# Performance work log

Hardware: AMD Instinct MI355X
Metric: run time of the kernel (lower is better)

Reference implementation:

```python
import jax, jax.numpy as jnp
import numpy as np

B, S, H = 8, 1024, 1024
NH, DH = 16, 64
F_DIM, E, TOPK = 4096, 8, 2
EPS = 1e-5


def setup_inputs() -> dict:
    key = jax.random.key(0)
    ks = jax.random.split(key, 12)
    s = 0.02
    return {
        "x": jax.random.normal(ks[0], (B, S, H), jnp.float32),
        "ln1_w": jnp.ones((H,), jnp.float32),
        "ln1_b": jnp.zeros((H,), jnp.float32),
        "ln2_w": jnp.ones((H,), jnp.float32),
        "ln2_b": jnp.zeros((H,), jnp.float32),
        "in_proj_w": jax.random.normal(ks[1], (3 * H, H), jnp.float32) * s,
        "in_proj_b": jnp.zeros((3 * H,), jnp.float32),
        "out_proj_w": jax.random.normal(ks[2], (H, H), jnp.float32) * s,
        "out_proj_b": jnp.zeros((H,), jnp.float32),
        "gate_w": jax.random.normal(ks[3], (E, H), jnp.float32) * s,
        "gate_b": jnp.zeros((E,), jnp.float32),
        "w1": jax.random.normal(ks[4], (E, H, F_DIM), jnp.float32) * s,
        "b1": jnp.zeros((E, F_DIM), jnp.float32),
        "w2": jax.random.normal(ks[5], (E, F_DIM, H), jnp.float32) * s,
        "b2": jnp.zeros((E, H), jnp.float32),
    }


def _layernorm(x, w, b):
    mu = jnp.mean(x, axis=-1, keepdims=True)
    var = jnp.var(x, axis=-1, keepdims=True)
    return (x - mu) * jax.lax.rsqrt(var + EPS) * w + b


def reference(x, ln1_w, ln1_b, ln2_w, ln2_b, in_proj_w, in_proj_b,
              out_proj_w, out_proj_b, gate_w, gate_b, w1, b1, w2, b2):
    # --- attention sub-block ---
    xn = _layernorm(x, ln1_w, ln1_b)
    qkv = xn @ in_proj_w.T + in_proj_b                     # [B,S,3H]
    q, k, v = jnp.split(qkv, 3, axis=-1)
    q = q.reshape(B, S, NH, DH).transpose(0, 2, 1, 3)      # [B,NH,S,DH]
    k = k.reshape(B, S, NH, DH).transpose(0, 2, 1, 3)
    v = v.reshape(B, S, NH, DH).transpose(0, 2, 1, 3)
    scores = jnp.einsum("bhqd,bhkd->bhqk", q, k) / jnp.sqrt(jnp.float32(DH))
    attn = jax.nn.softmax(scores, axis=-1)
    ctx = jnp.einsum("bhqk,bhkd->bhqd", attn, v)
    ctx = ctx.transpose(0, 2, 1, 3).reshape(B, S, H)
    x = x + ctx @ out_proj_w.T + out_proj_b

    # --- MoE sub-block (dense compute-all-experts, top-k combine) ---
    xn2 = _layernorm(x, ln2_w, ln2_b)
    logits = xn2 @ gate_w.T + gate_b                       # [B,S,E]
    topk_vals, topk_idx = jax.lax.top_k(logits, TOPK)      # [B,S,K]
    probs = jax.nn.softmax(topk_vals, axis=-1)
    hid = jax.nn.gelu(jnp.einsum("bsh,ehf->bsef", xn2, w1) + b1, approximate=False)
    expert_out = jnp.einsum("bsef,efh->bseh", hid, w2) + b2  # [B,S,E,H]
    selected = jnp.take_along_axis(expert_out, topk_idx[..., None], axis=2)  # [B,S,K,H]
    moe_out = jnp.sum(probs[..., None] * selected, axis=2)
    return x + moe_out
```

## Files before the change

kernel.cpp:

```cpp
#include <hip/hip_runtime.h>
#include <math.h>

typedef unsigned short u16;
typedef short short8 __attribute__((ext_vector_type(8)));
typedef float f32x4 __attribute__((ext_vector_type(4)));
typedef unsigned short us4 __attribute__((ext_vector_type(4)));

#define NTOK 8192
#define NEXP 8

__device__ __forceinline__ u16 f2bf(float f) {
  union { float f; unsigned u; } v; v.f = f;
  unsigned r = v.u + 0x7FFFu + ((v.u >> 16) & 1u);
  return (u16)(r >> 16);
}
__device__ __forceinline__ float bf2f(u16 u) {
  union { unsigned u; float f; } v; v.u = ((unsigned)u) << 16; return v.f;
}
__device__ __forceinline__ void gload16(const u16* src, u16* ldsDst) {
  __builtin_amdgcn_global_load_lds(
    (const __attribute__((address_space(1))) unsigned int*)(const void*)src,
    (__attribute__((address_space(3))) unsigned int*)(void*)ldsDst, 16, 0, 0);
}

__global__ void cast_kernel(const float* __restrict__ in, u16* __restrict__ out, int n4) {
  int i = blockIdx.x * blockDim.x + threadIdx.x;
  if (i < n4) {
    float4 v = ((const float4*)in)[i];
    us4 o;
    o[0] = f2bf(v.x); o[1] = f2bf(v.y); o[2] = f2bf(v.z); o[3] = f2bf(v.w);
    ((us4*)out)[i] = o;
  }
}

__global__ void transpose_cast(const float* __restrict__ in, u16* __restrict__ out, int R, int C) {
  __shared__ float tile[64][65];
  const size_t eoff = (size_t)blockIdx.z * (size_t)R * (size_t)C;
  in += eoff; out += eoff;
  const int rb = blockIdx.y * 64, cb = blockIdx.x * 64;
  const int tid = threadIdx.x;
  const int lr4 = tid >> 4;
  const int lc4 = (tid & 15) * 4;
#pragma unroll
  for (int p = 0; p < 4; ++p) {
    float4 v = *(const float4*)&in[(size_t)(rb + p * 16 + lr4) * C + cb + lc4];
    tile[p * 16 + lr4][lc4 + 0] = v.x;
    tile[p * 16 + lr4][lc4 + 1] = v.y;
    tile[p * 16 + lr4][lc4 + 2] = v.z;
    tile[p * 16 + lr4][lc4 + 3] = v.w;
  }
  __syncthreads();
  const int oc = tid >> 3;
  const int orr = (tid & 7) * 8;
#pragma unroll
  for (int p = 0; p < 2; ++p) {
    int c = p * 32 + oc;
    short8 o;
#pragma unroll
    for (int j = 0; j < 8; ++j) o[j] = (short)f2bf(tile[orr + j][c]);
    *(short8*)&out[(size_t)(cb + c) * R + rb + orr] = o;
  }
}

__global__ void ln1_kernel(const float* __restrict__ x, const float* __restrict__ w,
                           const float* __restrict__ b, u16* __restrict__ xn) {
  const int t = blockIdx.x, tid = threadIdx.x;
  __shared__ float red[8];
  float4 v = ((const float4*)(x + (size_t)t * 1024))[tid];
  float s  = v.x + v.y + v.z + v.w;
  float sq = v.x*v.x + v.y*v.y + v.z*v.z + v.w*v.w;
#pragma unroll
  for (int m = 1; m < 64; m <<= 1) { s += __shfl_xor(s, m, 64); sq += __shfl_xor(sq, m, 64); }
  if ((tid & 63) == 0) { red[tid >> 6] = s; red[4 + (tid >> 6)] = sq; }
  __syncthreads();
  float S = red[0] + red[1] + red[2] + red[3];
  float Q = red[4] + red[5] + red[6] + red[7];
  float mu  = S * (1.0f / 1024.0f);
  float var = Q * (1.0f / 1024.0f) - mu * mu;
  float inv = rsqrtf(var + 1e-5f);
  float4 wv = ((const float4*)w)[tid];
  float4 bv = ((const float4*)b)[tid];
  us4 o;
  o[0] = f2bf((v.x - mu) * inv * wv.x + bv.x);
  o[1] = f2bf((v.y - mu) * inv * wv.y + bv.y);
  o[2] = f2bf((v.z - mu) * inv * wv.z + bv.z);
  o[3] = f2bf((v.w - mu) * inv * wv.w + bv.w);
  ((us4*)(xn + (size_t)t * 1024))[tid] = o;
}

__global__ void ln2_gate_kernel(const float* __restrict__ x2, const float* __restrict__ w,
                                const float* __restrict__ b, const float* __restrict__ gw,
                                const float* __restrict__ gb, u16* __restrict__ xn2,
                                int* __restrict__ cnt, int* __restrict__ list_tok,
                                float* __restrict__ list_prob, int* __restrict__ tok2slot) {
  const int t = blockIdx.x, tid = threadIdx.x;
  __shared__ float red[8];
  __shared__ float logits[NEXP];
  __shared__ float xrow[1024];
  float4 v = ((const float4*)(x2 + (size_t)t * 1024))[tid];
  float s  = v.x + v.y + v.z + v.w;
  float sq = v.x*v.x + v.y*v.y + v.z*v.z + v.w*v.w;
#pragma unroll
  for (int m = 1; m < 64; m <<= 1) { s += __shfl_xor(s, m, 64); sq += __shfl_xor(sq, m, 64); }
  if ((tid & 63) == 0) { red[tid >> 6] = s; red[4 + (tid >> 6)] = sq; }
  __syncthreads();
  float S = red[0] + red[1] + red[2] + red[3];
  float Q = red[4] + red[5] + red[6] + red[7];
  float mu  = S * (1.0f / 1024.0f);
  float var = Q * (1.0f / 1024.0f) - mu * mu;
  float inv = rsqrtf(var + 1e-5f);
  float4 wv = ((const float4*)w)[tid];
  float4 bv = ((const float4*)b)[tid];
  float n0 = (v.x - mu) * inv * wv.x + bv.x;
  float n1 = (v.y - mu) * inv * wv.y + bv.y;
  float n2 = (v.z - mu) * inv * wv.z + bv.z;
  float n3 = (v.w - mu) * inv * wv.w + bv.w;
  xrow[tid*4+0] = n0; xrow[tid*4+1] = n1; xrow[tid*4+2] = n2; xrow[tid*4+3] = n3;
  us4 o; o[0] = f2bf(n0); o[1] = f2bf(n1); o[2] = f2bf(n2); o[3] = f2bf(n3);
  ((us4*)(xn2 + (size_t)t * 1024))[tid] = o;
  __syncthreads();
  int e = tid >> 5, l32 = tid & 31;
  const float* gwe = gw + e * 1024;
  float part = 0.0f;
  for (int i = l32; i < 1024; i += 32) part += xrow[i] * gwe[i];
#pragma unroll
  for (int m = 1; m < 32; m <<= 1) part += __shfl_xor(part, m, 64);
  if (l32 == 0) logits[e] = part + gb[e];
  __syncthreads();
  if (tid == 0) {
    float v0 = -1e30f; int e0 = 0;
#pragma unroll
    for (int i = 0; i < NEXP; ++i) { float L = logits[i]; if (L > v0) { v0 = L; e0 = i; } }
    float v1 = -1e30f; int e1 = 0;
#pragma unroll
    for (int i = 0; i < NEXP; ++i) { if (i == e0) continue; float L = logits[i]; if (L > v1) { v1 = L; e1 = i; } }
    float texp = expf(v1 - v0);
    float p0 = 1.0f / (1.0f + texp);
    float p1 = texp / (1.0f + texp);
    int s0 = atomicAdd(&cnt[e0], 1);
    list_tok[e0 * NTOK + s0] = t; list_prob[e0 * NTOK + s0] = p0;
    int s1 = atomicAdd(&cnt[e1], 1);
    list_tok[e1 * NTOK + s1] = t; list_prob[e1 * NTOK + s1] = p1;
    if (tok2slot) {
      tok2slot[2 * t]     = e0 * NTOK + s0;
      tok2slot[2 * t + 1] = e1 * NTOK + s1;
    }
  }
}

__launch_bounds__(256)
__global__ void attn_kernel(const u16* __restrict__ qkv, u16* __restrict__ ctx) {
  const int bh = blockIdx.y;
  const int b = bh >> 4, h = bh & 15;
  const int q0 = blockIdx.x * 64;
  const int tokBase = b * 1024;
  __shared__ __align__(16) u16 Qs[64 * 72];
  __shared__ __align__(16) u16 Ks[64 * 72];
  __shared__ __align__(16) u16 Vts[64 * 72];
  __shared__ __align__(16) u16 Ps[64 * 72];
  const int tid = threadIdx.x;
  const int wave = tid >> 6, lane = tid & 63, g = lane >> 4, lr = lane & 15;

  {
    int r = tid >> 2, d0 = (tid & 3) * 16;
    const u16* src = qkv + (size_t)(tokBase + q0 + r) * 3072 + h * 64 + d0;
    *(short8*)&Qs[r * 72 + d0]     = *(const short8*)src;
    *(short8*)&Qs[r * 72 + d0 + 8] = *(const short8*)(src + 8);
  }
  __syncthreads();
  short8 aq0 = *(const short8*)&Qs[(wave * 16 + lr) * 72 + g * 8];
  short8 aq1 = *(const short8*)&Qs[(wave * 16 + lr) * 72 + 32 + g * 8];

  const f32x4 zf = {0.f, 0.f, 0.f, 0.f};
  f32x4 Ofr[4] = {zf, zf, zf, zf};
  float m_run[4], l_run[4];
#pragma unroll
  for (int r = 0; r < 4; ++r) { m_run[r] = -1e30f; l_run[r] = 0.f; }

  for (int kt = 0; kt < 1024; kt += 64) {
    __syncthreads();
    {
      int r = tid >> 2, d0 = (tid & 3) * 16;
      const u16* ksrc = qkv + (size_t)(tokBase + kt + r) * 3072 + 1024 + h * 64 + d0;
      *(short8*)&Ks[r * 72 + d0]     = *(const short8*)ksrc;
      *(short8*)&Ks[r * 72 + d0 + 8] = *(const short8*)(ksrc + 8);
      const u16* vsrc = qkv + (size_t)(tokBase + kt + r) * 3072 + 2048 + h * 64 + d0;
      short8 v0 = *(const short8*)vsrc, v1 = *(const short8*)(vsrc + 8);
#pragma unroll
      for (int j = 0; j < 8; ++j) Vts[(d0 + j) * 72 + r] = (u16)v0[j];
#pragma unroll
      for (int j = 0; j < 8; ++j) Vts[(d0 + 8 + j) * 72 + r] = (u16)v1[j];
    }
    __syncthreads();
    f32x4 sf[4];
#pragma unroll
    for (int n = 0; n < 4; ++n) sf[n] = zf;
#pragma unroll
    for (int n = 0; n < 4; ++n) {
      short8 bk0 = *(const short8*)&Ks[(n * 16 + lr) * 72 + g * 8];
      short8 bk1 = *(const short8*)&Ks[(n * 16 + lr) * 72 + 32 + g * 8];
      sf[n] = __builtin_amdgcn_mfma_f32_16x16x32_bf16(aq0, bk0, sf[n], 0, 0, 0);
      sf[n] = __builtin_amdgcn_mfma_f32_16x16x32_bf16(aq1, bk1, sf[n], 0, 0, 0);
    }
#pragma unroll
    for (int n = 0; n < 4; ++n)
#pragma unroll
      for (int r = 0; r < 4; ++r) sf[n][r] *= 0.125f;
    float mnew[4], sc[4];
#pragma unroll
    for (int r = 0; r < 4; ++r) {
      float t0 = fmaxf(fmaxf(sf[0][r], sf[1][r]), fmaxf(sf[2][r], sf[3][r]));
#pragma unroll
      for (int msk = 1; msk < 16; msk <<= 1) t0 = fmaxf(t0, __shfl_xor(t0, msk, 64));
      mnew[r] = fmaxf(m_run[r], t0);
      sc[r] = __expf(m_run[r] - mnew[r]);
      m_run[r] = mnew[r];
    }
#pragma unroll
    for (int n = 0; n < 4; ++n)
#pragma unroll
      for (int r = 0; r < 4; ++r) sf[n][r] = __expf(sf[n][r] - mnew[r]);
#pragma unroll
    for (int r = 0; r < 4; ++r) {
      float s0 = sf[0][r] + sf[1][r] + sf[2][r] + sf[3][r];
#pragma unroll
      for (int msk = 1; msk < 16; msk <<= 1) s0 += __shfl_xor(s0, msk, 64);
      l_run[r] = l_run[r] * sc[r] + s0;
    }
#pragma unroll
    for (int nd = 0; nd < 4; ++nd)
#pragma unroll
      for (int r = 0; r < 4; ++r) Ofr[nd][r] *= sc[r];
#pragma unroll
    for (int n = 0; n < 4; ++n)
#pragma unroll
      for (int r = 0; r < 4; ++r)
        Ps[(wave * 16 + g * 4 + r) * 72 + n * 16 + lr] = f2bf(sf[n][r]);
    __syncthreads();
    short8 ap0 = *(const short8*)&Ps[(wave * 16 + lr) * 72 + g * 8];
    short8 ap1 = *(const short8*)&Ps[(wave * 16 + lr) * 72 + 32 + g * 8];
#pragma unroll
    for (int nd = 0; nd < 4; ++nd) {
      short8 bv0 = *(const short8*)&Vts[(nd * 16 + lr) * 72 + g * 8];
      short8 bv1 = *(const short8*)&Vts[(nd * 16 + lr) * 72 + 32 + g * 8];
      Ofr[nd] = __builtin_amdgcn_mfma_f32_16x16x32_bf16(ap0, bv0, Ofr[nd], 0, 0, 0);
      Ofr[nd] = __builtin_amdgcn_mfma_f32_16x16x32_bf16(ap1, bv1, Ofr[nd], 0, 0, 0);
    }
  }
#pragma unroll
  for (int nd = 0; nd < 4; ++nd)
#pragma unroll
    for (int r = 0; r < 4; ++r) {
      int tok = tokBase + q0 + wave * 16 + g * 4 + r;
      int col = h * 64 + nd * 16 + lr;
      ctx[(size_t)tok * 1024 + col] = f2bf(Ofr[nd][r] / l_run[r]);
    }
}

template<int EPI>
__launch_bounds__(512, 2)
__global__ void gemm256(const u16* __restrict__ Abase, const u16* __restrict__ Bbase,
                        int K, int lda, int N, int ldc,
                        const float* __restrict__ bias,
                        const float* __restrict__ resid,
                        float* __restrict__ outF,
                        u16* __restrict__ outB,
                        const int* __restrict__ cnt,
                        const int* __restrict__ list_tok,
                        const float* __restrict__ list_prob) {
  const int gx = gridDim.x, gy = gridDim.y;
  int nwg = gx * gy * gridDim.z;
  int orig = blockIdx.x + blockIdx.y * gx + blockIdx.z * gx * gy;
  int q8 = nwg >> 3, r8 = nwg & 7, xcd = orig & 7, lid = orig >> 3;
  int wg = (xcd < r8 ? xcd * (q8 + 1) : r8 * (q8 + 1) + (xcd - r8) * q8) + lid;
  const int bz = wg / (gx * gy); int rem = wg - bz * gx * gy;
  const int n0 = (rem % gx) * 256;
  const int m0 = (rem / gx) * 256;
  const int e  = bz;

  int M = NTOK;
  int slotBase = 0;
  const u16* Bw = Bbase;
  const float* biasp = bias;
  if constexpr (EPI >= 2) {
    for (int j = 0; j < e; ++j) slotBase += cnt[j];
    M = cnt[e];
    if (m0 >= M) return;
    Bw += (size_t)e * (size_t)N * (size_t)K;
    biasp = bias + (size_t)e * N;
  }

  __shared__ __align__(16) u16 As[2 * 16384];
  __shared__ __align__(16) u16 Bs[2 * 16384];

  const int tid = threadIdx.x;
  const int wave = tid >> 6, lane = tid & 63, g = lane >> 4, lr = lane & 15;
  const int wm = wave >> 2, wn = wave & 3;

  size_t aoff[4], boff[4];
#pragma unroll
  for (int i = 0; i < 4; ++i) {
    int ci = i * 512 + tid;
    int row = ci >> 3, c = ci & 7;
    int lc = c ^ (row & 7);
    int arow;
    if constexpr (EPI == 2) {
      int ridx = m0 + row; if (ridx > M - 1) ridx = M - 1;
      arow = list_tok[e * NTOK + ridx];
    } else if constexpr (EPI >= 3) {
      int ridx = m0 + row; if (ridx > M - 1) ridx = M - 1;
      arow = slotBase + ridx;
    } else {
      arow = m0 + row;
    }
    aoff[i] = (size_t)arow * (size_t)lda + (size_t)(lc << 3);
    boff[i] = (size_t)(n0 + row) * (size_t)K + (size_t)(lc << 3);
  }

  const int NT = K >> 6;

#define STAGE(T) do { int _t = (T); if (_t < NT) { int _b = (_t & 1) << 14; int _kt = _t << 6; \
    _Pragma("unroll") for (int i = 0; i < 4; ++i) \
      gload16(Abase + aoff[i] + _kt, &As[_b + ((i * 512 + wave * 64) << 3)]); \
    _Pragma("unroll") for (int i = 0; i < 4; ++i) \
      gload16(Bw + boff[i] + _kt, &Bs[_b + ((i * 512 + wave * 64) << 3)]); } } while (0)

  const int sw = lr & 7;
  const int abase = (wm * 128 + lr) * 64;
  const int bbase = (wn * 64 + lr) * 64;
  const int sk0 = (g ^ sw) * 8;
  const int sk1 = ((4 + g) ^ sw) * 8;

  const f32x4 zf = {0.f, 0.f, 0.f, 0.f};
  f32x4 acc[8][4];
#pragma unroll
  for (int m = 0; m < 8; ++m)
#pragma unroll
    for (int n = 0; n < 4; ++n) acc[m][n] = zf;

  STAGE(0);
  STAGE(1);

  for (int t = 0; t < NT; ++t) {
    if (t < NT - 1) { asm volatile("s_waitcnt vmcnt(8)" ::: "memory"); }
    else           { asm volatile("s_waitcnt vmcnt(0)" ::: "memory"); }
    __builtin_amdgcn_s_barrier();
    asm volatile("" ::: "memory");
    const u16* Ab = As + ((t & 1) << 14);
    const u16* Bb = Bs + ((t & 1) << 14);
    short8 bfr[2][4];
#pragma unroll
    for (int n = 0; n < 4; ++n) bfr[0][n] = *(const short8*)&Bb[bbase + n * 1024 + sk0];
#pragma unroll
    for (int n = 0; n < 4; ++n) bfr[1][n] = *(const short8*)&Bb[bbase + n * 1024 + sk1];
    short8 afr[8];
#pragma unroll
    for (int m = 0; m < 8; ++m) afr[m] = *(const short8*)&Ab[abase + m * 1024 + sk0];
    __builtin_amdgcn_s_setprio(1);
#pragma unroll
    for (int m = 0; m < 8; ++m)
#pragma unroll
      for (int n = 0; n < 4; ++n)
        acc[m][n] = __builtin_amdgcn_mfma_f32_16x16x32_bf16(afr[m], bfr[0][n], acc[m][n], 0, 0, 0);
    __builtin_amdgcn_s_setprio(0);
#pragma unroll
    for (int m = 0; m < 8; ++m) afr[m] = *(const short8*)&Ab[abase + m * 1024 + sk1];
    asm volatile("s_waitcnt lgkmcnt(0)" ::: "memory");
    __builtin_amdgcn_s_barrier();
    asm volatile("" ::: "memory");
    STAGE(t + 2);
    __builtin_amdgcn_s_setprio(1);
#pragma unroll
    for (int m = 0; m < 8; ++m)
#pragma unroll
      for (int n = 0; n < 4; ++n)
        acc[m][n] = __builtin_amdgcn_mfma_f32_16x16x32_bf16(afr[m], bfr[1][n], acc[m][n], 0, 0, 0);
    __builtin_amdgcn_s_setprio(0);
  }
#undef STAGE

#pragma unroll
  for (int m = 0; m < 8; ++m) {
    int rloc = wm * 128 + m * 16 + g * 4;
#pragma unroll
    for (int n = 0; n < 4; ++n) {
      int gc = n0 + wn * 64 + n * 16 + lr;
      float bcol = biasp[gc];
#pragma unroll
      for (int r = 0; r < 4; ++r) {
        int ridx = m0 + rloc + r;
        float vv = acc[m][n][r] + bcol;
        if constexpr (EPI == 0) {
          outB[(size_t)ridx * ldc + gc] = f2bf(vv);
        } else if constexpr (EPI == 1) {
          size_t off = (size_t)ridx * ldc + gc;
          outF[off] = vv + resid[off];
        } else if constexpr (EPI == 2) {
          if (ridx < M)
            outB[(size_t)(slotBase + ridx) * ldc + gc] =
              f2bf(0.5f * vv * (1.0f + erff(vv * 0.70710678f)));
        } else if constexpr (EPI == 3) {
          if (ridx < M)
            outB[(size_t)(slotBase + ridx) * ldc + gc] = f2bf(vv);
        } else {
          if (ridx < M) {
            int tok = list_tok[e * NTOK + ridx];
            float p = list_prob[e * NTOK + ridx];
            atomicAdd(&outF[(size_t)tok * ldc + gc], vv * p);
          }
        }
      }
    }
  }
}

__global__ void combine_kernel(const u16* __restrict__ part, const int* __restrict__ cnt,
                               const int* __restrict__ tok2slot, const float* __restrict__ lprb,
                               float* __restrict__ out) {
  const int t = blockIdx.x, tid = threadIdx.x;
  __shared__ int base[NEXP];
  if (tid == 0) {
    int b = 0;
#pragma unroll
    for (int j = 0; j < NEXP; ++j) { base[j] = b; b += cnt[j]; }
  }
  __syncthreads();
  int c0 = tok2slot[2 * t], c1 = tok2slot[2 * t + 1];
  float p0 = lprb[c0], p1 = lprb[c1];
  int g0 = base[c0 >> 13] + (c0 & 8191);
  int g1 = base[c1 >> 13] + (c1 & 8191);
  us4 a = ((const us4*)(part + (size_t)g0 * 1024))[tid];
  us4 b = ((const us4*)(part + (size_t)g1 * 1024))[tid];
  float4 o = ((const float4*)(out + (size_t)t * 1024))[tid];
  o.x += p0 * bf2f(a[0]) + p1 * bf2f(b[0]);
  o.y += p0 * bf2f(a[1]) + p1 * bf2f(b[1]);
  o.z += p0 * bf2f(a[2]) + p1 * bf2f(b[2]);
  o.w += p0 * bf2f(a[3]) + p1 * bf2f(b[3]);
  ((float4*)(out + (size_t)t * 1024))[tid] = o;
}

extern "C" void kernel_launch(void* const* d_in, const int* in_sizes, int n_in,
                              void* d_out, int out_size, void* d_ws, size_t ws_size,
                              hipStream_t stream) {
  const float* x    = (const float*)d_in[0];
  const float* ln1w = (const float*)d_in[1];
  const float* ln1b = (const float*)d_in[2];
  const float* ln2w = (const float*)d_in[3];
  const float* ln2b = (const float*)d_in[4];
  const float* inw  = (const float*)d_in[5];
  const float* inb  = (const float*)d_in[6];
  const float* outw = (const float*)d_in[7];
  const float* outb = (const float*)d_in[8];
  const float* gw   = (const float*)d_in[9];
  const float* gb   = (const float*)d_in[10];
  const float* w1   = (const float*)d_in[11];
  const float* b1   = (const float*)d_in[12];
  const float* w2   = (const float*)d_in[13];
  const float* b2   = (const float*)d_in[14];
  float* out = (float*)d_out;
  char* ws = (char*)d_ws;

  u16* xn1 = (u16*)(ws + 0);
  u16* qkv = (u16*)(ws + 16777216);
  u16* ctx = (u16*)(ws + 67108864);
  u16* hid = (u16*)(ws + 0);
  u16* xn2 = (u16*)(ws + 134217728);
  u16* w1t = (u16*)(ws + 150994944);
  u16* winb  = (u16*)(ws + 218103808);
  u16* woutb = (u16*)(ws + 224395264);
  u16* w2t = (u16*)(ws + 134217728);
  u16* part = (u16*)(ws + 201326592);

  const bool bigWS = ws_size >= 235471872ull;
  int*   cnt, *ltok, *t2s; float* lprb;
  if (bigWS) {
    cnt  = (int*)(ws + 234881024);
    ltok = (int*)(ws + 234882048);
    lprb = (float*)(ws + 235144192);
    t2s  = (int*)(ws + 235406336);
  } else {
    cnt  = (int*)(ws + 226492416);
    ltok = (int*)(ws + 226492672);
    lprb = (float*)(ws + 226754816);
    t2s  = nullptr;
  }

  cast_kernel<<<3072, 256, 0, stream>>>(inw, winb, 786432);
  cast_kernel<<<1024, 256, 0, stream>>>(outw, woutb, 262144);
  transpose_cast<<<dim3(64, 16, 8), 256, 0, stream>>>(w1, w1t, 1024, 4096);

  ln1_kernel<<<8192, 256, 0, stream>>>(x, ln1w, ln1b, xn1);
  gemm256<0><<<dim3(12, 32, 1), 512, 0, stream>>>(xn1, winb, 1024, 1024, 3072, 3072,
                                                  inb, nullptr, nullptr, qkv, nullptr, nullptr, nullptr);
  attn_kernel<<<dim3(16, 128), 256, 0, stream>>>(qkv, ctx);
  gemm256<1><<<dim3(4, 32, 1), 512, 0, stream>>>(ctx, woutb, 1024, 1024, 1024, 1024,
                                                 outb, x, out, nullptr, nullptr, nullptr, nullptr);

  hipMemsetAsync(cnt, 0, 32, stream);
  ln2_gate_kernel<<<8192, 256, 0, stream>>>(out, ln2w, ln2b, gw, gb, xn2, cnt, ltok, lprb, t2s);
  gemm256<2><<<dim3(16, 32, 8), 512, 0, stream>>>(xn2, w1t, 1024, 1024, 4096, 4096,
                                                  b1, nullptr, nullptr, hid, cnt, ltok, lprb);
  transpose_cast<<<dim3(16, 64, 8), 256, 0, stream>>>(w2, w2t, 4096, 1024);
  if (bigWS) {
    gemm256<3><<<dim3(4, 32, 8), 512, 0, stream>>>(hid, w2t, 4096, 4096, 1024, 1024,
                                                   b2, nullptr, nullptr, part, cnt, ltok, lprb);
    combine_kernel<<<8192, 256, 0, stream>>>(part, cnt, t2s, lprb, out);
  } else {
    gemm256<4><<<dim3(4, 32, 8), 512, 0, stream>>>(hid, w2t, 4096, 4096, 1024, 1024,
                                                   b2, nullptr, out, nullptr, cnt, ltok, lprb);
  }
}
```

Measured before the change: 1.082 ms.

## Switch to 128x128 GEMM tiles with compacted expert tile schedule and fast GELU

Replaces the 256x256, 512-thread GEMM with a 128x128, 256-thread tile kernel that uses a simpler double-buffered loop. A new plan kernel builds a compact list of (expert, row-block) tiles so the MoE GEMMs launch only populated tiles instead of a full 8-expert grid with early exits. The exact erf GELU is replaced by a polynomial erf approximation using fast reciprocal and exp. Smaller tiles raise occupancy and cut padding waste for uneven expert counts, but they lower per-tile data reuse and change the pipeline depth. Offsets also drop from 64-bit to 32-bit.

```diff
diff --git a/kernel.cpp b/kernel.cpp
--- a/kernel.cpp
+++ b/kernel.cpp
@@ -21,6 +21,15 @@
   __builtin_amdgcn_global_load_lds(
     (const __attribute__((address_space(1))) unsigned int*)(const void*)src,
     (__attribute__((address_space(3))) unsigned int*)(void*)ldsDst, 16, 0, 0);
+}
+__device__ __forceinline__ float gelu_f(float v) {
+  float ax = fabsf(v) * 0.70710678f;
+  float t = __builtin_amdgcn_rcpf(1.0f + 0.3275911f * ax);
+  float p = t * (0.254829592f + t * (-0.284496736f + t * (1.421413741f +
+            t * (-1.453152027f + t * 1.061405429f))));
+  float er = 1.0f - p * __expf(-ax * ax);
+  er = copysignf(er, v);
+  return 0.5f * v * (1.0f + er);
 }
 
 __global__ void cast_kernel(const float* __restrict__ in, u16* __restrict__ out, int n4) {
@@ -148,6 +157,20 @@
   }
 }
 
+__global__ void plan_kernel(const int* __restrict__ cnt, int* __restrict__ meta) {
+  if (threadIdx.x == 0) {
+    int base = 0, p = 0;
+    for (int e = 0; e < NEXP; ++e) {
+      meta[e] = base;
+      int c = cnt[e];
+      base += c;
+      int nm = (c + 127) >> 7;
+      for (int i = 0; i < nm; ++i) { meta[16 + 2 * p] = e; meta[17 + 2 * p] = i << 7; ++p; }
+    }
+    meta[8] = p;
+  }
+}
+
 __launch_bounds__(256)
 __global__ void attn_kernel(const u16* __restrict__ qkv, u16* __restrict__ ctx) {
   const int bh = blockIdx.y;
@@ -258,49 +281,51 @@
 }
 
 template<int EPI>
-__launch_bounds__(512, 2)
-__global__ void gemm256(const u16* __restrict__ Abase, const u16* __restrict__ Bbase,
+__launch_bounds__(256)
+__global__ void gemm128(const u16* __restrict__ Abase, const u16* __restrict__ Bbase,
                         int K, int lda, int N, int ldc,
                         const float* __restrict__ bias,
                         const float* __restrict__ resid,
                         float* __restrict__ outF,
                         u16* __restrict__ outB,
                         const int* __restrict__ cnt,
+                        const int* __restrict__ meta,
                         const int* __restrict__ list_tok,
                         const float* __restrict__ list_prob) {
   const int gx = gridDim.x, gy = gridDim.y;
-  int nwg = gx * gy * gridDim.z;
-  int orig = blockIdx.x + blockIdx.y * gx + blockIdx.z * gx * gy;
+  int nwg = gx * gy;
+  int orig = blockIdx.x + blockIdx.y * gx;
   int q8 = nwg >> 3, r8 = nwg & 7, xcd = orig & 7, lid = orig >> 3;
   int wg = (xcd < r8 ? xcd * (q8 + 1) : r8 * (q8 + 1) + (xcd - r8) * q8) + lid;
-  const int bz = wg / (gx * gy); int rem = wg - bz * gx * gy;
-  const int n0 = (rem % gx) * 256;
-  const int m0 = (rem / gx) * 256;
-  const int e  = bz;
-
-  int M = NTOK;
-  int slotBase = 0;
+  const int bx = wg % gx, by = wg / gx;
+  const int n0 = bx * 128;
+
+  int m0, e = 0, M = NTOK, slotBase = 0;
   const u16* Bw = Bbase;
   const float* biasp = bias;
   if constexpr (EPI >= 2) {
-    for (int j = 0; j < e; ++j) slotBase += cnt[j];
+    if (by >= meta[8]) return;
+    e = meta[16 + 2 * by];
+    m0 = meta[17 + 2 * by];
     M = cnt[e];
-    if (m0 >= M) return;
+    slotBase = meta[e];
     Bw += (size_t)e * (size_t)N * (size_t)K;
     biasp = bias + (size_t)e * N;
-  }
-
-  __shared__ __align__(16) u16 As[2 * 16384];
-  __shared__ __align__(16) u16 Bs[2 * 16384];
+  } else {
+    m0 = by * 128;
+  }
+
+  __shared__ __align__(16) u16 As[2][8192];
+  __shared__ __align__(16) u16 Bs[2][8192];
 
   const int tid = threadIdx.x;
   const int wave = tid >> 6, lane = tid & 63, g = lane >> 4, lr = lane & 15;
-  const int wm = wave >> 2, wn = wave & 3;
-
-  size_t aoff[4], boff[4];
+  const int wm = wave >> 1, wn = wave & 1;
+
+  unsigned aoff[4], boff[4];
 #pragma unroll
   for (int i = 0; i < 4; ++i) {
-    int ci = i * 512 + tid;
+    int ci = i * 256 + tid;
     int row = ci >> 3, c = ci & 7;
     int lc = c ^ (row & 7);
     int arow;
@@ -313,75 +338,66 @@
     } else {
       arow = m0 + row;
     }
-    aoff[i] = (size_t)arow * (size_t)lda + (size_t)(lc << 3);
-    boff[i] = (size_t)(n0 + row) * (size_t)K + (size_t)(lc << 3);
+    aoff[i] = (unsigned)arow * (unsigned)lda + (unsigned)(lc << 3);
+    boff[i] = (unsigned)(n0 + row) * (unsigned)K + (unsigned)(lc << 3);
   }
 
   const int NT = K >> 6;
 
-#define STAGE(T) do { int _t = (T); if (_t < NT) { int _b = (_t & 1) << 14; int _kt = _t << 6; \
-    _Pragma("unroll") for (int i = 0; i < 4; ++i) \
-      gload16(Abase + aoff[i] + _kt, &As[_b + ((i * 512 + wave * 64) << 3)]); \
-    _Pragma("unroll") for (int i = 0; i < 4; ++i) \
-      gload16(Bw + boff[i] + _kt, &Bs[_b + ((i * 512 + wave * 64) << 3)]); } } while (0)
+#define STAGE(T) do { int _t = (T); if (_t < NT) { int _b = _t & 1; int _kt = _t << 6; \
+    _Pragma("unroll") for (int i = 0; i < 4; ++i) { \
+      gload16(Abase + aoff[i] + _kt, &As[_b][(i * 256 + wave * 64) << 3]); \
+      gload16(Bw + boff[i] + _kt, &Bs[_b][(i * 256 + wave * 64) << 3]); } } } while (0)
 
   const int sw = lr & 7;
-  const int abase = (wm * 128 + lr) * 64;
-  const int bbase = (wn * 64 + lr) * 64;
+  const int arb = (wm * 64 + lr) * 64;
+  const int brb = (wn * 64 + lr) * 64;
   const int sk0 = (g ^ sw) * 8;
   const int sk1 = ((4 + g) ^ sw) * 8;
 
   const f32x4 zf = {0.f, 0.f, 0.f, 0.f};
-  f32x4 acc[8][4];
-#pragma unroll
-  for (int m = 0; m < 8; ++m)
+  f32x4 acc[4][4];
+#pragma unroll
+  for (int m = 0; m < 4; ++m)
 #pragma unroll
     for (int n = 0; n < 4; ++n) acc[m][n] = zf;
 
   STAGE(0);
-  STAGE(1);
+  asm volatile("s_waitcnt vmcnt(0)" ::: "memory");
+  __builtin_amdgcn_s_barrier();
 
   for (int t = 0; t < NT; ++t) {
-    if (t < NT - 1) { asm volatile("s_waitcnt vmcnt(8)" ::: "memory"); }
-    else           { asm volatile("s_waitcnt vmcnt(0)" ::: "memory"); }
+    STAGE(t + 1);
+    const u16* Ab = As[t & 1];
+    const u16* Bb = Bs[t & 1];
+    short8 af[4][2], bf[4][2];
+#pragma unroll
+    for (int m = 0; m < 4; ++m) {
+      af[m][0] = *(const short8*)&Ab[arb + m * 1024 + sk0];
+      af[m][1] = *(const short8*)&Ab[arb + m * 1024 + sk1];
+    }
+#pragma unroll
+    for (int n = 0; n < 4; ++n) {
+      bf[n][0] = *(const short8*)&Bb[brb + n * 1024 + sk0];
+      bf[n][1] = *(const short8*)&Bb[brb + n * 1024 + sk1];
+    }
+    __builtin_amdgcn_s_setprio(1);
+#pragma unroll
+    for (int kk = 0; kk < 2; ++kk)
+#pragma unroll
+      for (int m = 0; m < 4; ++m)
+#pragma unroll
+        for (int n = 0; n < 4; ++n)
+          acc[m][n] = __builtin_amdgcn_mfma_f32_16x16x32_bf16(af[m][kk], bf[n][kk], acc[m][n], 0, 0, 0);
+    __builtin_amdgcn_s_setprio(0);
+    asm volatile("s_waitcnt vmcnt(0)" ::: "memory");
     __builtin_amdgcn_s_barrier();
-    asm volatile("" ::: "memory");
-    const u16* Ab = As + ((t & 1) << 14);
-    const u16* Bb = Bs + ((t & 1) << 14);
-    short8 bfr[2][4];
-#pragma unroll
-    for (int n = 0; n < 4; ++n) bfr[0][n] = *(const short8*)&Bb[bbase + n * 1024 + sk0];
-#pragma unroll
-    for (int n = 0; n < 4; ++n) bfr[1][n] = *(const short8*)&Bb[bbase + n * 1024 + sk1];
-    short8 afr[8];
-#pragma unroll
-    for (int m = 0; m < 8; ++m) afr[m] = *(const short8*)&Ab[abase + m * 1024 + sk0];
-    __builtin_amdgcn_s_setprio(1);
-#pragma unroll
-    for (int m = 0; m < 8; ++m)
-#pragma unroll
-      for (int n = 0; n < 4; ++n)
-        acc[m][n] = __builtin_amdgcn_mfma_f32_16x16x32_bf16(afr[m], bfr[0][n], acc[m][n], 0, 0, 0);
-    __builtin_amdgcn_s_setprio(0);
-#pragma unroll
-    for (int m = 0; m < 8; ++m) afr[m] = *(const short8*)&Ab[abase + m * 1024 + sk1];
-    asm volatile("s_waitcnt lgkmcnt(0)" ::: "memory");
-    __builtin_amdgcn_s_barrier();
-    asm volatile("" ::: "memory");
-    STAGE(t + 2);
-    __builtin_amdgcn_s_setprio(1);
-#pragma unroll
-    for (int m = 0; m < 8; ++m)
-#pragma unroll
-      for (int n = 0; n < 4; ++n)
-        acc[m][n] = __builtin_amdgcn_mfma_f32_16x16x32_bf16(afr[m], bfr[1][n], acc[m][n], 0, 0, 0);
-    __builtin_amdgcn_s_setprio(0);
   }
 #undef STAGE
 
 #pragma unroll
-  for (int m = 0; m < 8; ++m) {
-    int rloc = wm * 128 + m * 16 + g * 4;
+  for (int m = 0; m < 4; ++m) {
+    int rloc = wm * 64 + m * 16 + g * 4;
 #pragma unroll
     for (int n = 0; n < 4; ++n) {
       int gc = n0 + wn * 64 + n * 16 + lr;
@@ -397,8 +413,7 @@
           outF[off] = vv + resid[off];
         } else if constexpr (EPI == 2) {
           if (ridx < M)
-            outB[(size_t)(slotBase + ridx) * ldc + gc] =
-              f2bf(0.5f * vv * (1.0f + erff(vv * 0.70710678f)));
+            outB[(size_t)(slotBase + ridx) * ldc + gc] = f2bf(gelu_f(vv));
         } else if constexpr (EPI == 3) {
           if (ridx < M)
             outB[(size_t)(slotBase + ridx) * ldc + gc] = f2bf(vv);
@@ -471,17 +486,19 @@
   u16* w2t = (u16*)(ws + 134217728);
   u16* part = (u16*)(ws + 201326592);
 
-  const bool bigWS = ws_size >= 235471872ull;
-  int*   cnt, *ltok, *t2s; float* lprb;
+  const bool bigWS = ws_size >= 235475456ull;
+  int *cnt, *meta, *ltok, *t2s; float* lprb;
   if (bigWS) {
     cnt  = (int*)(ws + 234881024);
-    ltok = (int*)(ws + 234882048);
-    lprb = (float*)(ws + 235144192);
-    t2s  = (int*)(ws + 235406336);
+    meta = (int*)(ws + 234883072);
+    ltok = (int*)(ws + 234887168);
+    lprb = (float*)(ws + 235149312);
+    t2s  = (int*)(ws + 235411456);
   } else {
     cnt  = (int*)(ws + 226492416);
-    ltok = (int*)(ws + 226492672);
-    lprb = (float*)(ws + 226754816);
+    meta = (int*)(ws + 226494464);
+    ltok = (int*)(ws + 226498560);
+    lprb = (float*)(ws + 226760704);
     t2s  = nullptr;
   }
 
@@ -490,23 +507,24 @@
   transpose_cast<<<dim3(64, 16, 8), 256, 0, stream>>>(w1, w1t, 1024, 4096);
 
   ln1_kernel<<<8192, 256, 0, stream>>>(x, ln1w, ln1b, xn1);
-  gemm256<0><<<dim3(12, 32, 1), 512, 0, stream>>>(xn1, winb, 1024, 1024, 3072, 3072,
-                                                  inb, nullptr, nullptr, qkv, nullptr, nullptr, nullptr);
+  gemm128<0><<<dim3(24, 64), 256, 0, stream>>>(xn1, winb, 1024, 1024, 3072, 3072,
+                                               inb, nullptr, nullptr, qkv, nullptr, nullptr, nullptr, nullptr);
   attn_kernel<<<dim3(16, 128), 256, 0, stream>>>(qkv, ctx);
-  gemm256<1><<<dim3(4, 32, 1), 512, 0, stream>>>(ctx, woutb, 1024, 1024, 1024, 1024,
-                                                 outb, x, out, nullptr, nullptr, nullptr, nullptr);
+  gemm128<1><<<dim3(8, 64), 256, 0, stream>>>(ctx, woutb, 1024, 1024, 1024, 1024,
+                                              outb, x, out, nullptr, nullptr, nullptr, nullptr, nullptr);
 
   hipMemsetAsync(cnt, 0, 32, stream);
   ln2_gate_kernel<<<8192, 256, 0, stream>>>(out, ln2w, ln2b, gw, gb, xn2, cnt, ltok, lprb, t2s);
-  gemm256<2><<<dim3(16, 32, 8), 512, 0, stream>>>(xn2, w1t, 1024, 1024, 4096, 4096,
-                                                  b1, nullptr, nullptr, hid, cnt, ltok, lprb);
+  plan_kernel<<<1, 64, 0, stream>>>(cnt, meta);
+  gemm128<2><<<dim3(32, 136), 256, 0, stream>>>(xn2, w1t, 1024, 1024, 4096, 4096,
+                                                b1, nullptr, nullptr, hid, cnt, meta, ltok, lprb);
   transpose_cast<<<dim3(16, 64, 8), 256, 0, stream>>>(w2, w2t, 4096, 1024);
   if (bigWS) {
-    gemm256<3><<<dim3(4, 32, 8), 512, 0, stream>>>(hid, w2t, 4096, 4096, 1024, 1024,
-                                                   b2, nullptr, nullptr, part, cnt, ltok, lprb);
+    gemm128<3><<<dim3(8, 136), 256, 0, stream>>>(hid, w2t, 4096, 4096, 1024, 1024,
+                                                 b2, nullptr, nullptr, part, cnt, meta, ltok, lprb);
     combine_kernel<<<8192, 256, 0, stream>>>(part, cnt, t2s, lprb, out);
   } else {
-    gemm256<4><<<dim3(4, 32, 8), 512, 0, stream>>>(hid, w2t, 4096, 4096, 1024, 1024,
-                                                   b2, nullptr, out, nullptr, cnt, ltok, lprb);
-  }
-}
+    gemm128<4><<<dim3(8, 136), 256, 0, stream>>>(hid, w2t, 4096, 4096, 1024, 1024,
+                                                 b2, nullptr, out, nullptr, cnt, meta, ltok, lprb);
+  }
+}
```

After: 1.115 ms, median of 2. 1.03x slower.
